# Optimization experiments

Measured on AMD Instinct MI355X. Metric: run time of the kernel, lower is better.

Reference implementation:

```python
import jax, jax.numpy as jnp
import numpy as np
from jax import lax
from jax.scipy.special import logsumexp

NUM_TAGS = 5
B, L = 16384, 512


def setup_inputs() -> dict:
    key = jax.random.key(0)
    k1, k2, k3, k4, k5 = jax.random.split(key, 5)
    emissions = jax.random.normal(k1, (B, L, NUM_TAGS), dtype=jnp.float32)
    tags = jax.random.randint(k2, (B, L), 0, NUM_TAGS)
    mask = jnp.ones((B, L), dtype=bool)
    # learned CRF parameters, init U(-0.1, 0.1) as in reset_parameters
    transitions = jax.random.uniform(k3, (NUM_TAGS, NUM_TAGS), minval=-0.1, maxval=0.1, dtype=jnp.float32)
    start_transitions = jax.random.uniform(k4, (NUM_TAGS,), minval=-0.1, maxval=0.1, dtype=jnp.float32)
    end_transitions = jax.random.uniform(k5, (NUM_TAGS,), minval=-0.1, maxval=0.1, dtype=jnp.float32)
    return {
        "emissions": emissions,
        "transitions": transitions,
        "start_transitions": start_transitions,
        "end_transitions": end_transitions,
        "tags": tags,
        "mask": mask,
    }


def reference(emissions, transitions, start_transitions, end_transitions, tags, mask):
    """CRF mean negative log-likelihood: log_partition - gold_score (both batch means)."""
    Bs, Ls, C = emissions.shape
    maskf = mask.astype(emissions.dtype)

    # ---- log partition (forward algorithm); note: original torch code's
    # mask application here is a no-op (where(mask, s, s)), reproduced faithfully.
    init_score = start_transitions[None, :] + emissions[:, 0]  # (B, C)

    def step(score, em_i):
        # score: (B, C) over previous tag; em_i: (B, C)
        nxt = logsumexp(score[:, :, None] + transitions[None, :, :] + em_i[:, None, :], axis=1)
        return nxt, None

    ems = jnp.swapaxes(emissions[:, 1:], 0, 1)  # (L-1, B, C)
    final_score, _ = lax.scan(step, init_score, ems)
    log_den = logsumexp(final_score + end_transitions[None, :], axis=1).mean()

    # ---- gold path score (fully vectorized over time)
    s0 = start_transitions[tags[:, 0]] + jnp.take_along_axis(emissions[:, 0], tags[:, :1], axis=1)[:, 0]
    trans_scores = transitions[tags[:, :-1], tags[:, 1:]]  # (B, L-1)
    em_at_tags = jnp.take_along_axis(emissions, tags[:, :, None], axis=2)[:, :, 0]  # (B, L)
    path_score = s0 + ((trans_scores + em_at_tags[:, 1:]) * maskf[:, 1:]).sum(axis=1)
    last_idx = mask.sum(axis=1).astype(jnp.int32) - 1  # (B,)
    last_tags = jnp.take_along_axis(tags, last_idx[:, None], axis=1)[:, 0]
    log_num = (path_score + end_transitions[last_tags]).mean()

    return log_den - log_num
```

## Files before the change

kernel.cpp:

```cpp
#include <hip/hip_runtime.h>

#define NTAGS 5
#define BATCH 16384
#define SEQL 512
#define NCHUNK 8
#define CHUNKL 64
#define TT 8
#define NTILE (CHUNKL / TT)
#define RECF 32

__device__ __forceinline__ float f4c(float4 v, int c) {
    switch (c & 3) { case 0: return v.x; case 1: return v.y; case 2: return v.z; default: return v.w; }
}
__device__ __forceinline__ int i4c(int4 v, int c) {
    switch (c & 3) { case 0: return v.x; case 1: return v.y; case 2: return v.z; default: return v.w; }
}
__device__ __forceinline__ float sel5v(float a0, float a1, float a2, float a3, float a4, int t) {
    float r = a0;
    r = (t == 1) ? a1 : r;
    r = (t == 2) ? a2 : r;
    r = (t == 3) ? a3 : r;
    r = (t == 4) ? a4 : r;
    return r;
}

struct P1State {
    float M[25];
    float logS;
    float path;
    int prev;
};

__device__ __forceinline__ void p1_tile(const float4* tb, const int4* tg, bool sk0,
                                        P1State& st, const float eT[25],
                                        const float* ldsT, const float stR[5]) {
#pragma unroll
    for (int t = 0; t < TT; ++t) {
#define EMX(j) f4c(tb[(t * 5 + (j)) >> 2], (t * 5 + (j)) & 3)
        const float e0 = EMX(0), e1 = EMX(1), e2 = EMX(2), e3 = EMX(3), e4 = EMX(4);
#undef EMX
        const int tag = i4c(tg[t >> 2], t & 3);
        if (sk0 && t == 0) {
            st.path += sel5v(stR[0], stR[1], stR[2], stR[3], stR[4], tag) +
                       sel5v(e0, e1, e2, e3, e4, tag);
            st.prev = tag;
        } else {
            const float ex0 = __expf(e0), ex1 = __expf(e1), ex2 = __expf(e2),
                        ex3 = __expf(e3), ex4 = __expf(e4);
#pragma unroll
            for (int i = 0; i < 5; ++i) {
                const float m0 = st.M[i * 5 + 0], m1 = st.M[i * 5 + 1], m2 = st.M[i * 5 + 2],
                            m3 = st.M[i * 5 + 3], m4 = st.M[i * 5 + 4];
#pragma unroll
                for (int j = 0; j < 5; ++j) {
                    float a = m0 * eT[j];
                    a = fmaf(m1, eT[5 + j], a);
                    a = fmaf(m2, eT[10 + j], a);
                    a = fmaf(m3, eT[15 + j], a);
                    a = fmaf(m4, eT[20 + j], a);
                    const float exj = (j == 0) ? ex0 : (j == 1) ? ex1 : (j == 2) ? ex2
                                     : (j == 3) ? ex3 : ex4;
                    st.M[i * 5 + j] = a * exj;
                }
            }
            st.path += ldsT[st.prev * 5 + tag] + sel5v(e0, e1, e2, e3, e4, tag);
            st.prev = tag;
        }
        if ((t & 3) == 3) {
            float m = st.M[0];
#pragma unroll
            for (int i = 1; i < 25; ++i) m = fmaxf(m, st.M[i]);
            st.logS += __logf(m);
            const float rc = __builtin_amdgcn_rcpf(m);
#pragma unroll
            for (int i = 0; i < 25; ++i) st.M[i] *= rc;
        }
    }
}

__global__ __launch_bounds__(256, 2) void crf_phase1(
    const float* __restrict__ emis, const float* __restrict__ trans,
    const float* __restrict__ startT, const int* __restrict__ tags,
    float* __restrict__ ws) {
    __shared__ float ldsT[25];
    const int tid = threadIdx.x;
    if (tid < 25) ldsT[tid] = trans[tid];
    __syncthreads();

    float eT[25];
#pragma unroll
    for (int i = 0; i < 25; ++i) eT[i] = __expf(trans[i]);
    float stR[5];
#pragma unroll
    for (int j = 0; j < 5; ++j) stR[j] = startT[j];

    const int gt = blockIdx.x * 256 + tid;
    const int seq = gt >> 3;
    const int chunk = gt & 7;
    const bool first = (chunk == 0);

    const float4* esrc =
        (const float4*)(emis + (size_t)seq * (SEQL * NTAGS) + chunk * (CHUNKL * NTAGS));
    const int tbase = seq * SEQL + chunk * CHUNKL;
    const int4* tsrc = (const int4*)(tags + tbase);

    P1State st;
#pragma unroll
    for (int i = 0; i < 25; ++i) st.M[i] = 0.f;
    st.M[0] = st.M[6] = st.M[12] = st.M[18] = st.M[24] = 1.f;
    st.logS = 0.f;
    st.path = 0.f;
    st.prev = 0;
    if (!first) st.prev = tags[tbase - 1];

    float4 tA[10], tB[10];
    int4 gA[2], gB[2];
#pragma unroll
    for (int k = 0; k < 10; ++k) tA[k] = esrc[k];
    gA[0] = tsrc[0];
    gA[1] = tsrc[1];

#pragma unroll 1
    for (int tp = 0; tp < NTILE; tp += 2) {
        {
            const float4* ep = esrc + (tp + 1) * 10;
#pragma unroll
            for (int k = 0; k < 10; ++k) tB[k] = ep[k];
            const int4* tq = tsrc + (tp + 1) * 2;
            gB[0] = tq[0];
            gB[1] = tq[1];
        }
        p1_tile(tA, gA, first && (tp == 0), st, eT, ldsT, stR);
        {
            const int nx = (tp + 2 < NTILE) ? tp + 2 : tp;
            const float4* ep = esrc + nx * 10;
#pragma unroll
            for (int k = 0; k < 10; ++k) tA[k] = ep[k];
            const int4* tq = tsrc + nx * 2;
            gA[0] = tq[0];
            gA[1] = tq[1];
        }
        p1_tile(tB, gB, false, st, eT, ldsT, stR);
    }

    float4* rec = (float4*)(ws + (size_t)gt * RECF);
#pragma unroll
    for (int k = 0; k < 6; ++k)
        rec[k] = make_float4(st.M[4 * k], st.M[4 * k + 1], st.M[4 * k + 2], st.M[4 * k + 3]);
    rec[6] = make_float4(st.M[24], st.logS, st.path, 0.f);
}

__device__ __forceinline__ void p2_combine(const float4 r[7], float v[5], float& logZ,
                                           float& path) {
#define MM(i, j) f4c(r[((i) * 5 + (j)) >> 2], ((i) * 5 + (j)) & 3)
    float nv[5];
#pragma unroll
    for (int j = 0; j < 5; ++j) {
        float a = v[0] * MM(0, j);
        a = fmaf(v[1], MM(1, j), a);
        a = fmaf(v[2], MM(2, j), a);
        a = fmaf(v[3], MM(3, j), a);
        a = fmaf(v[4], MM(4, j), a);
        nv[j] = a;
    }
#undef MM
    logZ += r[6].y;
    path += r[6].z;
    const float m = fmaxf(fmaxf(fmaxf(nv[0], nv[1]), fmaxf(nv[2], nv[3])), nv[4]);
    logZ += __logf(m);
    const float rc = __builtin_amdgcn_rcpf(m);
#pragma unroll
    for (int j = 0; j < 5; ++j) v[j] = nv[j] * rc;
}

__global__ __launch_bounds__(256, 1) void crf_phase2(
    const float* __restrict__ emis, const float* __restrict__ startT,
    const float* __restrict__ endT, const int* __restrict__ tags,
    const float* __restrict__ ws, float* __restrict__ out) {
    const int seq = blockIdx.x * 256 + threadIdx.x;
    const float* eb = emis + (size_t)seq * (SEQL * NTAGS);
    const float4 e03 = *(const float4*)eb;
    const float e4v = eb[4];
    const float s0 = startT[0] + e03.x, s1 = startT[1] + e03.y, s2 = startT[2] + e03.z,
                s3 = startT[3] + e03.w, s4 = startT[4] + e4v;
    const float m0 = fmaxf(fmaxf(fmaxf(s0, s1), fmaxf(s2, s3)), s4);
    float v[5] = {__expf(s0 - m0), __expf(s1 - m0), __expf(s2 - m0), __expf(s3 - m0),
                  __expf(s4 - m0)};
    float logZ = m0, path = 0.f;

    const float4* wsb = (const float4*)(ws + (size_t)seq * NCHUNK * RECF);
    float4 rA[7], rB[7];
#pragma unroll
    for (int k = 0; k < 7; ++k) rA[k] = wsb[k];

#pragma unroll 1
    for (int c = 0; c < NCHUNK; c += 2) {
#pragma unroll
        for (int k = 0; k < 7; ++k) rB[k] = wsb[(c + 1) * 8 + k];
        p2_combine(rA, v, logZ, path);
        const int nx = (c + 2 < NCHUNK) ? c + 2 : c;
#pragma unroll
        for (int k = 0; k < 7; ++k) rA[k] = wsb[nx * 8 + k];
        p2_combine(rB, v, logZ, path);
    }

    const float en0 = endT[0], en1 = endT[1], en2 = endT[2], en3 = endT[3], en4 = endT[4];
    float sden = v[0] * __expf(en0);
    sden = fmaf(v[1], __expf(en1), sden);
    sden = fmaf(v[2], __expf(en2), sden);
    sden = fmaf(v[3], __expf(en3), sden);
    sden = fmaf(v[4], __expf(en4), sden);
    const float den = logZ + __logf(sden);

    const int lastTag = tags[seq * SEQL + (SEQL - 1)];
    const float num = path + sel5v(en0, en1, en2, en3, en4, lastTag);

    float val = (den - num) * (1.0f / (float)BATCH);
#pragma unroll
    for (int off = 32; off > 0; off >>= 1) val += __shfl_xor(val, off, 64);
    if ((threadIdx.x & 63) == 0) atomicAdd(out, val);
}

extern "C" void kernel_launch(void* const* d_in, const int* in_sizes, int n_in,
                              void* d_out, int out_size, void* d_ws, size_t ws_size,
                              hipStream_t stream) {
    const float* emis = (const float*)d_in[0];
    const float* trans = (const float*)d_in[1];
    const float* startT = (const float*)d_in[2];
    const float* endT = (const float*)d_in[3];
    const int* tags = (const int*)d_in[4];
    float* out = (float*)d_out;
    float* ws = (float*)d_ws;

    hipMemsetAsync(out, 0, sizeof(float), stream);
    crf_phase1<<<dim3(BATCH * NCHUNK / 256), dim3(256), 0, stream>>>(emis, trans, startT,
                                                                     tags, ws);
    crf_phase2<<<dim3(BATCH / 256), dim3(256), 0, stream>>>(emis, startT, endT, tags, ws,
                                                            out);
}
```

Before: 313.7 us.

## Split sequences into 16 chunks with smaller tiles and higher occupancy

Phase 1 now uses 16 time chunks per sequence when the workspace is large enough, doubling the thread-level parallelism of the matrix-product scan. Tiles shrink to 4 steps with a single int4 tag load, the transition gathers are hoisted out of the step loop, and launch bounds ask for 4 waves per SIMD to reduce register pressure and raise occupancy. Phase 2 combines twice as many chunk records per sequence using 64-thread blocks so more blocks spread across CUs. The cost is more workspace traffic and a longer serial combine in phase 2, and the compiler may spill registers to meet the tighter occupancy bound.

```diff
diff --git a/kernel.cpp b/kernel.cpp
--- a/kernel.cpp
+++ b/kernel.cpp
@@ -3,10 +3,7 @@
 #define NTAGS 5
 #define BATCH 16384
 #define SEQL 512
-#define NCHUNK 8
-#define CHUNKL 64
-#define TT 8
-#define NTILE (CHUNKL / TT)
+#define TT 4
 #define RECF 32
 
 __device__ __forceinline__ float f4c(float4 v, int c) {
@@ -31,19 +28,24 @@
     int prev;
 };
 
-__device__ __forceinline__ void p1_tile(const float4* tb, const int4* tg, bool sk0,
+__device__ __forceinline__ void p1_tile(const float4 tb[5], const int4 tg, bool sk0,
                                         P1State& st, const float eT[25],
                                         const float* ldsT, const float stR[5]) {
+    const int t0 = i4c(tg, 0), t1 = i4c(tg, 1), t2 = i4c(tg, 2), t3 = i4c(tg, 3);
+    float trv[4];
+    trv[0] = ldsT[st.prev * 5 + t0];
+    trv[1] = ldsT[t0 * 5 + t1];
+    trv[2] = ldsT[t1 * 5 + t2];
+    trv[3] = ldsT[t2 * 5 + t3];
 #pragma unroll
     for (int t = 0; t < TT; ++t) {
 #define EMX(j) f4c(tb[(t * 5 + (j)) >> 2], (t * 5 + (j)) & 3)
         const float e0 = EMX(0), e1 = EMX(1), e2 = EMX(2), e3 = EMX(3), e4 = EMX(4);
 #undef EMX
-        const int tag = i4c(tg[t >> 2], t & 3);
+        const int tag = (t == 0) ? t0 : (t == 1) ? t1 : (t == 2) ? t2 : t3;
+        const float emtag = sel5v(e0, e1, e2, e3, e4, tag);
         if (sk0 && t == 0) {
-            st.path += sel5v(stR[0], stR[1], stR[2], stR[3], stR[4], tag) +
-                       sel5v(e0, e1, e2, e3, e4, tag);
-            st.prev = tag;
+            st.path += sel5v(stR[0], stR[1], stR[2], stR[3], stR[4], tag) + emtag;
         } else {
             const float ex0 = __expf(e0), ex1 = __expf(e1), ex2 = __expf(e2),
                         ex3 = __expf(e3), ex4 = __expf(e4);
@@ -63,25 +65,26 @@
                     st.M[i * 5 + j] = a * exj;
                 }
             }
-            st.path += ldsT[st.prev * 5 + tag] + sel5v(e0, e1, e2, e3, e4, tag);
-            st.prev = tag;
+            st.path += trv[t] + emtag;
         }
-        if ((t & 3) == 3) {
-            float m = st.M[0];
-#pragma unroll
-            for (int i = 1; i < 25; ++i) m = fmaxf(m, st.M[i]);
-            st.logS += __logf(m);
-            const float rc = __builtin_amdgcn_rcpf(m);
-#pragma unroll
-            for (int i = 0; i < 25; ++i) st.M[i] *= rc;
-        }
-    }
-}
-
-__global__ __launch_bounds__(256, 2) void crf_phase1(
+        st.prev = tag;
+    }
+    float m = st.M[0];
+#pragma unroll
+    for (int i = 1; i < 25; ++i) m = fmaxf(m, st.M[i]);
+    st.logS += __logf(m);
+    const float rc = __builtin_amdgcn_rcpf(m);
+#pragma unroll
+    for (int i = 0; i < 25; ++i) st.M[i] *= rc;
+}
+
+template <int NCHUNK>
+__global__ __launch_bounds__(256, 4) void crf_phase1(
     const float* __restrict__ emis, const float* __restrict__ trans,
     const float* __restrict__ startT, const int* __restrict__ tags,
     float* __restrict__ ws) {
+    constexpr int CHUNKL = SEQL / NCHUNK;
+    constexpr int NTILE = CHUNKL / TT;
     __shared__ float ldsT[25];
     const int tid = threadIdx.x;
     if (tid < 25) ldsT[tid] = trans[tid];
@@ -95,8 +98,8 @@
     for (int j = 0; j < 5; ++j) stR[j] = startT[j];
 
     const int gt = blockIdx.x * 256 + tid;
-    const int seq = gt >> 3;
-    const int chunk = gt & 7;
+    const int seq = gt / NCHUNK;
+    const int chunk = gt % NCHUNK;
     const bool first = (chunk == 0);
 
     const float4* esrc =
@@ -110,35 +113,29 @@
     st.M[0] = st.M[6] = st.M[12] = st.M[18] = st.M[24] = 1.f;
     st.logS = 0.f;
     st.path = 0.f;
-    st.prev = 0;
-    if (!first) st.prev = tags[tbase - 1];
-
-    float4 tA[10], tB[10];
-    int4 gA[2], gB[2];
-#pragma unroll
-    for (int k = 0; k < 10; ++k) tA[k] = esrc[k];
-    gA[0] = tsrc[0];
-    gA[1] = tsrc[1];
+    st.prev = first ? 0 : tags[tbase - 1];
+
+    float4 tA[5], tB[5];
+    int4 gA, gB;
+#pragma unroll
+    for (int k = 0; k < 5; ++k) tA[k] = esrc[k];
+    gA = tsrc[0];
 
 #pragma unroll 1
     for (int tp = 0; tp < NTILE; tp += 2) {
         {
-            const float4* ep = esrc + (tp + 1) * 10;
-#pragma unroll
-            for (int k = 0; k < 10; ++k) tB[k] = ep[k];
-            const int4* tq = tsrc + (tp + 1) * 2;
-            gB[0] = tq[0];
-            gB[1] = tq[1];
+            const float4* ep = esrc + (tp + 1) * 5;
+#pragma unroll
+            for (int k = 0; k < 5; ++k) tB[k] = ep[k];
+            gB = tsrc[tp + 1];
         }
         p1_tile(tA, gA, first && (tp == 0), st, eT, ldsT, stR);
         {
             const int nx = (tp + 2 < NTILE) ? tp + 2 : tp;
-            const float4* ep = esrc + nx * 10;
-#pragma unroll
-            for (int k = 0; k < 10; ++k) tA[k] = ep[k];
-            const int4* tq = tsrc + nx * 2;
-            gA[0] = tq[0];
-            gA[1] = tq[1];
+            const float4* ep = esrc + nx * 5;
+#pragma unroll
+            for (int k = 0; k < 5; ++k) tA[k] = ep[k];
+            gA = tsrc[nx];
         }
         p1_tile(tB, gB, false, st, eT, ldsT, stR);
     }
@@ -173,11 +170,12 @@
     for (int j = 0; j < 5; ++j) v[j] = nv[j] * rc;
 }
 
-__global__ __launch_bounds__(256, 1) void crf_phase2(
+template <int NCHUNK>
+__global__ __launch_bounds__(64, 1) void crf_phase2(
     const float* __restrict__ emis, const float* __restrict__ startT,
     const float* __restrict__ endT, const int* __restrict__ tags,
     const float* __restrict__ ws, float* __restrict__ out) {
-    const int seq = blockIdx.x * 256 + threadIdx.x;
+    const int seq = blockIdx.x * 64 + threadIdx.x;
     const float* eb = emis + (size_t)seq * (SEQL * NTAGS);
     const float4 e03 = *(const float4*)eb;
     const float e4v = eb[4];
@@ -218,7 +216,7 @@
     float val = (den - num) * (1.0f / (float)BATCH);
 #pragma unroll
     for (int off = 32; off > 0; off >>= 1) val += __shfl_xor(val, off, 64);
-    if ((threadIdx.x & 63) == 0) atomicAdd(out, val);
+    if (threadIdx.x == 0) atomicAdd(out, val);
 }
 
 extern "C" void kernel_launch(void* const* d_in, const int* in_sizes, int n_in,
@@ -233,8 +231,16 @@
     float* ws = (float*)d_ws;
 
     hipMemsetAsync(out, 0, sizeof(float), stream);
-    crf_phase1<<<dim3(BATCH * NCHUNK / 256), dim3(256), 0, stream>>>(emis, trans, startT,
-                                                                     tags, ws);
-    crf_phase2<<<dim3(BATCH / 256), dim3(256), 0, stream>>>(emis, startT, endT, tags, ws,
-                                                            out);
-}
+    const size_t need16 = (size_t)BATCH * 16 * RECF * sizeof(float);
+    if (ws_size >= need16) {
+        crf_phase1<16><<<dim3(BATCH * 16 / 256), dim3(256), 0, stream>>>(emis, trans,
+                                                                         startT, tags, ws);
+        crf_phase2<16><<<dim3(BATCH / 64), dim3(64), 0, stream>>>(emis, startT, endT,
+                                                                  tags, ws, out);
+    } else {
+        crf_phase1<8><<<dim3(BATCH * 8 / 256), dim3(256), 0, stream>>>(emis, trans,
+                                                                       startT, tags, ws);
+        crf_phase2<8><<<dim3(BATCH / 64), dim3(64), 0, stream>>>(emis, startT, endT,
+                                                                 tags, ws, out);
+    }
+}
```

Measured after the change: 534.9 us. 1.71x slower.
